# Performance work log

Hardware: AMD Instinct MI355X
Metric: run time of the kernel (lower is better)

Reference implementation:

```python
import math
import jax, jax.numpy as jnp
import numpy as np

BASE = 10000.0
SCALING_FACTOR = 1.0
ORIG_MAX_POS = 4096
BETA_FAST, BETA_SLOW = 32, 1
MSCALE = 0.707
MSCALE_ALL_DIM = 0.707


def _yarn_cos_sin(seq_len: int, dim: int):
    # DeepseekV3YarnRotaryEmbedding._set_cos_sin_cache, computed in numpy (constants)
    def corr_dim(num_rot):
        return dim * math.log(ORIG_MAX_POS / (num_rot * 2 * math.pi)) / (2 * math.log(BASE))
    low = max(math.floor(corr_dim(BETA_FAST)), 0)
    high = min(math.ceil(corr_dim(BETA_SLOW)), dim - 1)
    hi = high + 0.001 if low == high else high
    ramp = np.clip((np.arange(dim // 2, dtype=np.float32) - low) / (hi - low), 0.0, 1.0)
    inv_freq_mask = 1.0 - ramp
    freq_extra = 1.0 / BASE ** (np.arange(0, dim, 2, dtype=np.float32) / dim)
    freq_inter = freq_extra / SCALING_FACTOR
    inv_freq = freq_inter * (1.0 - inv_freq_mask) + freq_extra * inv_freq_mask
    t = np.arange(seq_len, dtype=np.float32)
    freqs = np.outer(t, inv_freq)
    def get_mscale(s, m):
        return 1.0 if s <= 1 else 0.1 * m * math.log(s) + 1.0
    _m = get_mscale(SCALING_FACTOR, MSCALE) / get_mscale(SCALING_FACTOR, MSCALE_ALL_DIM)
    emb = np.concatenate([freqs, freqs], axis=-1)  # [S, dim]
    return jnp.asarray(np.cos(emb) * _m), jnp.asarray(np.sin(emb) * _m)


def _rotate_half(x):
    x1, x2 = jnp.split(x, 2, axis=-1)
    return jnp.concatenate([-x2, x1], axis=-1)


def setup_inputs() -> dict:
    key = jax.random.key(0)
    ks = jax.random.split(key, 5)
    B, S, H, DN, DR, DV = 2, 2048, 16, 128, 64, 128
    return {
        "q_nope": jax.random.normal(ks[0], (B, S, H, DN), jnp.float32),
        "q_pe": jax.random.normal(ks[1], (B, S, H, DR), jnp.float32),
        "k_nope": jax.random.normal(ks[2], (B, S, H, DN), jnp.float32),
        "k_pe": jax.random.normal(ks[3], (B, S, 1, DR), jnp.float32),  # shared rope key head
        "v": jax.random.normal(ks[4], (B, S, H, DV), jnp.float32),
    }


def reference(q_nope, q_pe, k_nope, k_pe, v):
    B, S, H, DN = q_nope.shape
    DR = q_pe.shape[-1]
    sm_scale = (DN + DR) ** (-0.5)  # qk_head_dim**-0.5
    cos, sin = _yarn_cos_sin(S, DR)  # [S, DR]
    cos = cos[None, :, None, :]
    sin = sin[None, :, None, :]
    # decoupled RoPE on the rope slice (apply_rotary_pos_emb with position_ids=arange)
    qp = q_pe * cos + _rotate_half(q_pe) * sin              # [B,S,H,DR]
    kp = k_pe * cos + _rotate_half(k_pe) * sin              # [B,S,1,DR]
    kp = jnp.broadcast_to(kp, (B, S, H, DR))
    q = jnp.concatenate([q_nope, qp], axis=-1)              # [B,S,H,DN+DR]
    k = jnp.concatenate([k_nope, kp], axis=-1)
    # attention_ref: full fp32 logits, causal mask, lse*log2(e), softmax, PV
    logits = jnp.einsum('bmhd,bnhd->bhmn', q.astype(jnp.float32), k.astype(jnp.float32)) * sm_scale
    mask = jnp.arange(S)[:, None] >= jnp.arange(S)[None, :]  # qo_len == kv_len
    logits = jnp.where(mask[None, None], logits, -jnp.inf)
    lse = jnp.transpose(jax.scipy.special.logsumexp(logits, axis=-1), (0, 2, 1)) * math.log2(math.e)
    p = jax.nn.softmax(logits, axis=-1)
    o = jnp.einsum('bhmn,bnhd->bmhd', p, v.astype(jnp.float32))
    o = o.reshape(B * S, H, -1).astype(q_nope.dtype)        # [B*S, H, DV]
    return o, lse
```

## Files before the change

kernel.cpp:

```cpp
#include <hip/hip_runtime.h>
#include <hip/hip_bf16.h>
#include <math.h>

#define NB 2
#define SEQ 2048
#define NH 16
#define DNOPE 128
#define DROT 64
#define DVDIM 128
#define DQK 192
#define BM 64
#define BN 64

typedef __bf16 bf16x8_t __attribute__((ext_vector_type(8)));
typedef float f32x4_t __attribute__((ext_vector_type(4)));

#define LOG2_BASE_OVER_HALFDIM 0.41524101186092028f
#define KSL2 0.10412340175817158f
#define INV_2PI 0.15915494309189535f

#define KBF_ELEMS   ((size_t)NB * NH * SEQ * DQK)

#define KN_BLOCKS 4096
#define KR_BLOCKS 128
#define VPREP_BLOCKS 1024

__global__ __launch_bounds__(256) void prep_kernel(
    const float* __restrict__ k_nope, const float* __restrict__ k_pe,
    const float* __restrict__ v, __bf16* __restrict__ Kbf,
    __bf16* __restrict__ Vtb) {
  __shared__ __bf16 T[64][130];
  const int bid = blockIdx.x;
  const int tid = threadIdx.x;
  if (bid < KN_BLOCKS) {
    int gid = bid * 256 + tid;
    int d0 = (gid & 15) * 8;
    int rest = gid >> 4;
    int s = (rest >> 4) & (SEQ - 1);
    int h = rest & (NH - 1);
    int b = rest >> 15;
    const float* p = k_nope + ((size_t)((b * SEQ + s) * NH + h)) * DNOPE + d0;
    float4 a = *(const float4*)p;
    float4 c = *(const float4*)(p + 4);
    bf16x8_t o;
    o[0] = (__bf16)a.x; o[1] = (__bf16)a.y; o[2] = (__bf16)a.z; o[3] = (__bf16)a.w;
    o[4] = (__bf16)c.x; o[5] = (__bf16)c.y; o[6] = (__bf16)c.z; o[7] = (__bf16)c.w;
    *(bf16x8_t*)&Kbf[((size_t)(b * NH + h) * SEQ + s) * DQK + d0] = o;
  } else if (bid < KN_BLOCKS + KR_BLOCKS) {
    int gid = (bid - KN_BLOCKS) * 256 + tid;
    int dr0 = (gid & 7) * 8;
    int rest = gid >> 3;
    int s = rest & (SEQ - 1);
    int b = rest >> 11;
    const float* p = k_pe + (size_t)(b * SEQ + s) * DROT;
    float4 x0 = *(const float4*)(p + dr0);
    float4 x1 = *(const float4*)(p + dr0 + 4);
    int dro = (dr0 < 32) ? dr0 + 32 : dr0 - 32;
    float4 y0 = *(const float4*)(p + dro);
    float4 y1 = *(const float4*)(p + dro + 4);
    float sgn = (dr0 < 32) ? -1.0f : 1.0f;
    float xs[8] = {x0.x, x0.y, x0.z, x0.w, x1.x, x1.y, x1.z, x1.w};
    float ys[8] = {y0.x, y0.y, y0.z, y0.w, y1.x, y1.y, y1.z, y1.w};
    float invf0 = exp2f(-LOG2_BASE_OVER_HALFDIM * (float)(dr0 & 31));
    const float kj[8] = {
      1.0f,
      0.7499083907567589f,
      0.5624875938672282f,
      0.4219181499736729f,
      0.3163923045408737f,
      0.2372497216250197f,
      0.1779391804261401f,
      0.1334543036472316f};
    bf16x8_t o;
#pragma unroll
    for (int j = 0; j < 8; ++j) {
      float rev = (float)s * invf0 * (kj[j] * INV_2PI);
      rev = rev - floorf(rev);
      float sn = __builtin_amdgcn_sinf(rev);
      float cs = __builtin_amdgcn_cosf(rev);
      o[j] = (__bf16)(xs[j] * cs + sgn * ys[j] * sn);
    }
#pragma unroll
    for (int h = 0; h < NH; ++h)
      *(bf16x8_t*)&Kbf[((size_t)(b * NH + h) * SEQ + s) * DQK + DNOPE + dr0] = o;
  } else {
    int vb = bid - KN_BLOCKS - KR_BLOCKS;
    const int s0 = (vb & 31) * 64, h = (vb >> 5) & (NH - 1), b = vb >> 9;
#pragma unroll
    for (int r = 0; r < 8; ++r) {
      int task = tid + r * 256;
      int srow = task >> 5, c4 = (task & 31) * 4;
      const float* p = v + ((size_t)((b * SEQ + s0 + srow) * NH + h)) * DVDIM + c4;
      float4 a = *(const float4*)p;
      T[srow][c4 + 0] = (__bf16)a.x; T[srow][c4 + 1] = (__bf16)a.y;
      T[srow][c4 + 2] = (__bf16)a.z; T[srow][c4 + 3] = (__bf16)a.w;
    }
    __syncthreads();
#pragma unroll
    for (int r = 0; r < 4; ++r) {
      int task = tid + r * 256;
      int dv = task >> 3, c8 = (task & 7) * 8;
      bf16x8_t o;
#pragma unroll
      for (int u = 0; u < 8; ++u) o[u] = T[c8 + u][dv];
      *(bf16x8_t*)&Vtb[((size_t)(b * NH + h) * DVDIM + dv) * SEQ + s0 + c8] = o;
    }
  }
}

__global__ __launch_bounds__(256, 2) void mla_fwd_kernel(
    const float* __restrict__ q_nope, const float* __restrict__ q_pe,
    const __bf16* __restrict__ Kbf, const __bf16* __restrict__ Vtb,
    float* __restrict__ out_o, float* __restrict__ out_lse) {
  __shared__ __bf16 Kl[BN * DQK];
  __shared__ __bf16 Vl[DVDIM * BN];
  __shared__ __bf16 Pl[4 * 16 * BN];

  const int bx = blockIdx.x, h = blockIdx.y, b = blockIdx.z;
  const int tid = threadIdx.x;
  const int w = tid >> 6, lane = tid & 63;
  const int col = lane & 15, quad = lane >> 4;
  const int wm = w & 1;
  const int wnd = w >> 1;
  const int swz = col & 7;
  const int e0 = quad ^ swz, e1 = (quad + 4) ^ swz;

  const __bf16 onev = (col == 0) ? (__bf16)1.0f : (__bf16)0.0f;
  bf16x8_t vxf;
#pragma unroll
  for (int u = 0; u < 8; ++u) vxf[u] = onev;

  const __bf16* Kslab = Kbf + (size_t)(b * NH + h) * SEQ * DQK;
  const __bf16* Vslab = Vtb + (size_t)(b * NH + h) * DVDIM * SEQ;

  int kofs[6];
#pragma unroll
  for (int r = 0; r < 6; ++r) {
    int L = r * 256 + tid;
    int n = L / 24, jj = L - n * 24;
    int jsrc = (jj & ~7) | ((jj & 7) ^ (n & 7));
    kofs[r] = n * DQK + jsrc * 8;
  }
  int vofs[4];
#pragma unroll
  for (int r = 0; r < 4; ++r) {
    int L = r * 256 + tid;
    int dv = L >> 3, jj = L & 7;
    vofs[r] = dv * SEQ + (jj ^ (dv & 7)) * 8;
  }

  for (int half = 0; half < 2; ++half) {
    const int qt = half ? bx : (31 - bx);
    const int qb = qt * BM;

    bf16x8_t qf[2][6];
#pragma unroll
    for (int mt = 0; mt < 2; ++mt) {
      const int mrow = qb + wm * 32 + mt * 16 + col;
      const float* qn = q_nope + (size_t)((b * SEQ + mrow) * NH + h) * DNOPE;
      const float* qp = q_pe   + (size_t)((b * SEQ + mrow) * NH + h) * DROT;
#pragma unroll
      for (int c = 0; c < 4; ++c) {
        const float* p = qn + c * 32 + quad * 8;
        float4 a = *(const float4*)p;
        float4 bq = *(const float4*)(p + 4);
        bf16x8_t f;
        f[0]=(__bf16)(a.x*KSL2);  f[1]=(__bf16)(a.y*KSL2);
        f[2]=(__bf16)(a.z*KSL2);  f[3]=(__bf16)(a.w*KSL2);
        f[4]=(__bf16)(bq.x*KSL2); f[5]=(__bf16)(bq.y*KSL2);
        f[6]=(__bf16)(bq.z*KSL2); f[7]=(__bf16)(bq.w*KSL2);
        qf[mt][c] = f;
      }
      {
        const float* plo = qp + quad * 8;
        const float* phi = qp + 32 + quad * 8;
        float4 lo0 = *(const float4*)plo;
        float4 lo1 = *(const float4*)(plo + 4);
        float4 hi0 = *(const float4*)phi;
        float4 hi1 = *(const float4*)(phi + 4);
        float xl[8] = {lo0.x,lo0.y,lo0.z,lo0.w,lo1.x,lo1.y,lo1.z,lo1.w};
        float xh[8] = {hi0.x,hi0.y,hi0.z,hi0.w,hi1.x,hi1.y,hi1.z,hi1.w};
        bf16x8_t f4v, f5v;
#pragma unroll
        for (int j = 0; j < 8; ++j) {
          int i = quad * 8 + j;
          float invf = exp2f(-LOG2_BASE_OVER_HALFDIM * (float)i);
          float rev = (float)mrow * invf * INV_2PI;
          rev = rev - floorf(rev);
          float sn = __builtin_amdgcn_sinf(rev);
          float cs = __builtin_amdgcn_cosf(rev);
          f4v[j] = (__bf16)((xl[j] * cs - xh[j] * sn) * KSL2);
          f5v[j] = (__bf16)((xh[j] * cs + xl[j] * sn) * KSL2);
        }
        qf[mt][4] = f4v; qf[mt][5] = f5v;
      }
    }

    f32x4_t oacc[2][4];
#pragma unroll
    for (int mt = 0; mt < 2; ++mt)
#pragma unroll
      for (int d = 0; d < 4; ++d) oacc[mt][d] = (f32x4_t){0.f, 0.f, 0.f, 0.f};
    f32x4_t lacc[2];
    lacc[0] = (f32x4_t){0.f, 0.f, 0.f, 0.f};
    lacc[1] = (f32x4_t){0.f, 0.f, 0.f, 0.f};

    bf16x8_t Kreg[6], Vreg[4];
#pragma unroll
    for (int r = 0; r < 6; ++r) Kreg[r] = *(const bf16x8_t*)(Kslab + kofs[r]);
#pragma unroll
    for (int r = 0; r < 4; ++r) Vreg[r] = *(const bf16x8_t*)(Vslab + vofs[r]);

    for (int it = 0; it <= qt; ++it) {
      __syncthreads();
#pragma unroll
      for (int r = 0; r < 6; ++r) *(bf16x8_t*)&Kl[(r * 256 + tid) * 8] = Kreg[r];
#pragma unroll
      for (int r = 0; r < 4; ++r) *(bf16x8_t*)&Vl[(r * 256 + tid) * 8] = Vreg[r];
      __syncthreads();
      if (it < qt) {
        const __bf16* Ksrc = Kslab + (size_t)(it + 1) * BN * DQK;
        const __bf16* Vsrc = Vslab + (it + 1) * BN;
#pragma unroll
        for (int r = 0; r < 6; ++r) Kreg[r] = *(const bf16x8_t*)(Ksrc + kofs[r]);
#pragma unroll
        for (int r = 0; r < 4; ++r) Vreg[r] = *(const bf16x8_t*)(Vsrc + vofs[r]);
      }

      f32x4_t sacc[2][2];
#pragma unroll
      for (int mt = 0; mt < 2; ++mt)
#pragma unroll
        for (int nt = 0; nt < 2; ++nt) sacc[mt][nt] = (f32x4_t){0.f, 0.f, 0.f, 0.f};
#pragma unroll
      for (int nt = 0; nt < 2; ++nt) {
        const __bf16* kr = &Kl[(wnd * 32 + nt * 16 + col) * 24 * 8];
        bf16x8_t kf0 = *(const bf16x8_t*)&kr[e0 * 8];
        bf16x8_t kf1 = *(const bf16x8_t*)&kr[e1 * 8];
        bf16x8_t kf2 = *(const bf16x8_t*)&kr[64 + e0 * 8];
        bf16x8_t kf3 = *(const bf16x8_t*)&kr[64 + e1 * 8];
        bf16x8_t kf4 = *(const bf16x8_t*)&kr[128 + e0 * 8];
        bf16x8_t kf5 = *(const bf16x8_t*)&kr[128 + e1 * 8];
#pragma unroll
        for (int mt = 0; mt < 2; ++mt) {
          sacc[mt][nt] = __builtin_amdgcn_mfma_f32_16x16x32_bf16(qf[mt][0], kf0, sacc[mt][nt], 0, 0, 0);
          sacc[mt][nt] = __builtin_amdgcn_mfma_f32_16x16x32_bf16(qf[mt][1], kf1, sacc[mt][nt], 0, 0, 0);
          sacc[mt][nt] = __builtin_amdgcn_mfma_f32_16x16x32_bf16(qf[mt][2], kf2, sacc[mt][nt], 0, 0, 0);
          sacc[mt][nt] = __builtin_amdgcn_mfma_f32_16x16x32_bf16(qf[mt][3], kf3, sacc[mt][nt], 0, 0, 0);
          sacc[mt][nt] = __builtin_amdgcn_mfma_f32_16x16x32_bf16(qf[mt][4], kf4, sacc[mt][nt], 0, 0, 0);
          sacc[mt][nt] = __builtin_amdgcn_mfma_f32_16x16x32_bf16(qf[mt][5], kf5, sacc[mt][nt], 0, 0, 0);
        }
      }

      float pvv[2][2][4];
#pragma unroll
      for (int mt = 0; mt < 2; ++mt)
#pragma unroll
        for (int nt = 0; nt < 2; ++nt)
#pragma unroll
          for (int r = 0; r < 4; ++r) pvv[mt][nt][r] = exp2f(sacc[mt][nt][r]);
      if (it == qt) {
#pragma unroll
        for (int mt = 0; mt < 2; ++mt)
#pragma unroll
          for (int nt = 0; nt < 2; ++nt) {
            int nn = (it << 6) + wnd * 32 + nt * 16 + col;
#pragma unroll
            for (int r = 0; r < 4; ++r) {
              int mm = qb + wm * 32 + mt * 16 + quad * 4 + r;
              if (nn > mm) pvv[mt][nt][r] = 0.0f;
            }
          }
      }

#pragma unroll
      for (int mt = 0; mt < 2; ++mt) {
        __bf16* Pr = &Pl[(wm * 2 + mt) * 16 * BN];
#pragma unroll
        for (int nt = 0; nt < 2; ++nt)
#pragma unroll
          for (int r = 0; r < 4; ++r) {
            int row = quad * 4 + r;
            int j = wnd * 4 + nt * 2 + (col >> 3);
            Pr[(row * 8 + (j ^ (row & 7))) * 8 + (col & 7)] = (__bf16)pvv[mt][nt][r];
          }
      }
      __syncthreads();

      bf16x8_t pf0[2], pf1[2];
#pragma unroll
      for (int mt = 0; mt < 2; ++mt) {
        const __bf16* Pr = &Pl[(wm * 2 + mt) * 16 * BN];
        pf0[mt] = *(const bf16x8_t*)&Pr[(col * 8 + e0) * 8];
        pf1[mt] = *(const bf16x8_t*)&Pr[(col * 8 + e1) * 8];
      }
#pragma unroll
      for (int dt = 0; dt < 4; ++dt) {
        const __bf16* vr = &Vl[((wnd * 4 + dt) * 16 + col) * 64];
        bf16x8_t vf0 = *(const bf16x8_t*)&vr[e0 * 8];
        bf16x8_t vf1 = *(const bf16x8_t*)&vr[e1 * 8];
#pragma unroll
        for (int mt = 0; mt < 2; ++mt) {
          oacc[mt][dt] = __builtin_amdgcn_mfma_f32_16x16x32_bf16(pf0[mt], vf0, oacc[mt][dt], 0, 0, 0);
          oacc[mt][dt] = __builtin_amdgcn_mfma_f32_16x16x32_bf16(pf1[mt], vf1, oacc[mt][dt], 0, 0, 0);
        }
      }
#pragma unroll
      for (int mt = 0; mt < 2; ++mt) {
        lacc[mt] = __builtin_amdgcn_mfma_f32_16x16x32_bf16(pf0[mt], vxf, lacc[mt], 0, 0, 0);
        lacc[mt] = __builtin_amdgcn_mfma_f32_16x16x32_bf16(pf1[mt], vxf, lacc[mt], 0, 0, 0);
      }
    }

    float lr[2][4], inv_l[2][4];
#pragma unroll
    for (int mt = 0; mt < 2; ++mt)
#pragma unroll
      for (int r = 0; r < 4; ++r) {
        lr[mt][r] = __shfl(lacc[mt][r], lane & 48, 64);
        inv_l[mt][r] = 1.0f / lr[mt][r];
      }
#pragma unroll
    for (int mt = 0; mt < 2; ++mt)
#pragma unroll
      for (int dt = 0; dt < 4; ++dt)
#pragma unroll
        for (int r = 0; r < 4; ++r) {
          int mm = qb + wm * 32 + mt * 16 + quad * 4 + r;
          int dd = wnd * 64 + dt * 16 + col;
          out_o[(size_t)((b * SEQ + mm) * NH + h) * DVDIM + dd] =
              oacc[mt][dt][r] * inv_l[mt][r];
        }
    if (wnd == 0 && col < 4) {
#pragma unroll
      for (int mt = 0; mt < 2; ++mt) {
        int mm = qb + wm * 32 + mt * 16 + quad * 4 + col;
        out_lse[(size_t)(b * SEQ + mm) * NH + h] = log2f(lr[mt][col]);
      }
    }
  }
}

extern "C" void kernel_launch(void* const* d_in, const int* in_sizes, int n_in,
                              void* d_out, int out_size, void* d_ws, size_t ws_size,
                              hipStream_t stream) {
  const float* q_nope = (const float*)d_in[0];
  const float* q_pe   = (const float*)d_in[1];
  const float* k_nope = (const float*)d_in[2];
  const float* k_pe   = (const float*)d_in[3];
  const float* v      = (const float*)d_in[4];
  float* out_o   = (float*)d_out;
  float* out_lse = out_o + (size_t)NB * SEQ * NH * DVDIM;

  __bf16* Kbf = (__bf16*)d_ws;
  __bf16* Vtb = Kbf + KBF_ELEMS;

  prep_kernel<<<dim3(KN_BLOCKS + KR_BLOCKS + VPREP_BLOCKS), dim3(256), 0, stream>>>(
      k_nope, k_pe, v, Kbf, Vtb);
  mla_fwd_kernel<<<dim3(16, NH, NB), dim3(256), 0, stream>>>(
      q_nope, q_pe, Kbf, Vtb, out_o, out_lse);
}
```

Before: 232.2 us.

## Split PV over key halves per warp, removing mid-iteration block barrier

Each warp now multiplies its own 32-key slice of P by the full 128-wide V tile, using a private per-warp P buffer in shared memory. This removes the block-wide __syncthreads between writing and reading P in every KV iteration. The two partial O and row-sum accumulators are combined once at the end through a shared-memory reduction that reuses the K/V buffers. In exchange, O accumulator registers per thread double, which may raise register pressure or cause spills at two blocks per SM, and a reduction step with two extra barriers is added per query tile.

```diff
diff --git a/kernel.cpp b/kernel.cpp
--- a/kernel.cpp
+++ b/kernel.cpp
@@ -112,9 +112,12 @@
     const float* __restrict__ q_nope, const float* __restrict__ q_pe,
     const __bf16* __restrict__ Kbf, const __bf16* __restrict__ Vtb,
     float* __restrict__ out_o, float* __restrict__ out_lse) {
-  __shared__ __bf16 Kl[BN * DQK];
-  __shared__ __bf16 Vl[DVDIM * BN];
-  __shared__ __bf16 Pl[4 * 16 * BN];
+  __shared__ __align__(16) char smem[51200];
+  __bf16* Kl = (__bf16*)smem;
+  __bf16* Vl = (__bf16*)(smem + 24576);
+  __bf16* Pl = (__bf16*)(smem + 40960);
+  float*  Ored = (float*)smem;
+  float*  Lred = (float*)(smem + 64 * 132 * 4);
 
   const int bx = blockIdx.x, h = blockIdx.y, b = blockIdx.z;
   const int tid = threadIdx.x;
@@ -124,6 +127,7 @@
   const int wnd = w >> 1;
   const int swz = col & 7;
   const int e0 = quad ^ swz, e1 = (quad + 4) ^ swz;
+  const int ew = (wnd * 4 + quad) ^ swz;
 
   const __bf16 onev = (col == 0) ? (__bf16)1.0f : (__bf16)0.0f;
   bf16x8_t vxf;
@@ -148,6 +152,8 @@
     int dv = L >> 3, jj = L & 7;
     vofs[r] = dv * SEQ + (jj ^ (dv & 7)) * 8;
   }
+
+  __bf16* Pw = Pl + w * (32 * 40);
 
   for (int half = 0; half < 2; ++half) {
     const int qt = half ? bx : (31 - bx);
@@ -196,11 +202,11 @@
       }
     }
 
-    f32x4_t oacc[2][4];
+    f32x4_t oacc[2][8];
 #pragma unroll
     for (int mt = 0; mt < 2; ++mt)
 #pragma unroll
-      for (int d = 0; d < 4; ++d) oacc[mt][d] = (f32x4_t){0.f, 0.f, 0.f, 0.f};
+      for (int d = 0; d < 8; ++d) oacc[mt][d] = (f32x4_t){0.f, 0.f, 0.f, 0.f};
     f32x4_t lacc[2];
     lacc[0] = (f32x4_t){0.f, 0.f, 0.f, 0.f};
     lacc[1] = (f32x4_t){0.f, 0.f, 0.f, 0.f};
@@ -252,90 +258,84 @@
         }
       }
 
-      float pvv[2][2][4];
+      const bool dg = (it == qt);
 #pragma unroll
       for (int mt = 0; mt < 2; ++mt)
 #pragma unroll
         for (int nt = 0; nt < 2; ++nt)
 #pragma unroll
-          for (int r = 0; r < 4; ++r) pvv[mt][nt][r] = exp2f(sacc[mt][nt][r]);
-      if (it == qt) {
+          for (int r = 0; r < 4; ++r) {
+            float pe = exp2f(sacc[mt][nt][r]);
+            if (dg) {
+              int nn = (it << 6) + wnd * 32 + nt * 16 + col;
+              int mm = qb + wm * 32 + mt * 16 + quad * 4 + r;
+              if (nn > mm) pe = 0.0f;
+            }
+            Pw[(mt * 16 + quad * 4 + r) * 40 + nt * 16 + col] = (__bf16)pe;
+          }
+
+      bf16x8_t pa[2];
+#pragma unroll
+      for (int mt = 0; mt < 2; ++mt)
+        pa[mt] = *(const bf16x8_t*)&Pw[(mt * 16 + col) * 40 + quad * 8];
+#pragma unroll
+      for (int dt = 0; dt < 8; ++dt) {
+        bf16x8_t vf = *(const bf16x8_t*)&Vl[(dt * 16 + col) * 64 + ew * 8];
 #pragma unroll
         for (int mt = 0; mt < 2; ++mt)
-#pragma unroll
-          for (int nt = 0; nt < 2; ++nt) {
-            int nn = (it << 6) + wnd * 32 + nt * 16 + col;
-#pragma unroll
-            for (int r = 0; r < 4; ++r) {
-              int mm = qb + wm * 32 + mt * 16 + quad * 4 + r;
-              if (nn > mm) pvv[mt][nt][r] = 0.0f;
-            }
+          oacc[mt][dt] = __builtin_amdgcn_mfma_f32_16x16x32_bf16(pa[mt], vf, oacc[mt][dt], 0, 0, 0);
+      }
+#pragma unroll
+      for (int mt = 0; mt < 2; ++mt)
+        lacc[mt] = __builtin_amdgcn_mfma_f32_16x16x32_bf16(pa[mt], vxf, lacc[mt], 0, 0, 0);
+    }
+
+    __syncthreads();
+    if (wnd == 1) {
+#pragma unroll
+      for (int mt = 0; mt < 2; ++mt) {
+#pragma unroll
+        for (int dt = 0; dt < 8; ++dt)
+#pragma unroll
+          for (int r = 0; r < 4; ++r) {
+            int row = wm * 32 + mt * 16 + quad * 4 + r;
+            Ored[row * 132 + dt * 16 + col] = oacc[mt][dt][r];
           }
-      }
-
-#pragma unroll
-      for (int mt = 0; mt < 2; ++mt) {
-        __bf16* Pr = &Pl[(wm * 2 + mt) * 16 * BN];
-#pragma unroll
-        for (int nt = 0; nt < 2; ++nt)
+        if (col == 0)
+#pragma unroll
+          for (int r = 0; r < 4; ++r)
+            Lred[wm * 32 + mt * 16 + quad * 4 + r] = lacc[mt][r];
+      }
+    }
+    __syncthreads();
+    if (wnd == 0) {
+      float lr[2][4], inv_l[2][4];
+#pragma unroll
+      for (int mt = 0; mt < 2; ++mt)
+#pragma unroll
+        for (int r = 0; r < 4; ++r) {
+          float val = lacc[mt][r] + Lred[wm * 32 + mt * 16 + quad * 4 + r];
+          lr[mt][r] = __shfl(val, lane & 48, 64);
+          inv_l[mt][r] = 1.0f / lr[mt][r];
+        }
+#pragma unroll
+      for (int mt = 0; mt < 2; ++mt)
+#pragma unroll
+        for (int dt = 0; dt < 8; ++dt)
 #pragma unroll
           for (int r = 0; r < 4; ++r) {
-            int row = quad * 4 + r;
-            int j = wnd * 4 + nt * 2 + (col >> 3);
-            Pr[(row * 8 + (j ^ (row & 7))) * 8 + (col & 7)] = (__bf16)pvv[mt][nt][r];
+            int row = wm * 32 + mt * 16 + quad * 4 + r;
+            int mm = qb + row;
+            float sum = oacc[mt][dt][r] + Ored[row * 132 + dt * 16 + col];
+            out_o[(size_t)((b * SEQ + mm) * NH + h) * DVDIM + dt * 16 + col] =
+                sum * inv_l[mt][r];
           }
-      }
-      __syncthreads();
-
-      bf16x8_t pf0[2], pf1[2];
-#pragma unroll
-      for (int mt = 0; mt < 2; ++mt) {
-        const __bf16* Pr = &Pl[(wm * 2 + mt) * 16 * BN];
-        pf0[mt] = *(const bf16x8_t*)&Pr[(col * 8 + e0) * 8];
-        pf1[mt] = *(const bf16x8_t*)&Pr[(col * 8 + e1) * 8];
-      }
-#pragma unroll
-      for (int dt = 0; dt < 4; ++dt) {
-        const __bf16* vr = &Vl[((wnd * 4 + dt) * 16 + col) * 64];
-        bf16x8_t vf0 = *(const bf16x8_t*)&vr[e0 * 8];
-        bf16x8_t vf1 = *(const bf16x8_t*)&vr[e1 * 8];
+      if (col < 4) {
 #pragma unroll
         for (int mt = 0; mt < 2; ++mt) {
-          oacc[mt][dt] = __builtin_amdgcn_mfma_f32_16x16x32_bf16(pf0[mt], vf0, oacc[mt][dt], 0, 0, 0);
-          oacc[mt][dt] = __builtin_amdgcn_mfma_f32_16x16x32_bf16(pf1[mt], vf1, oacc[mt][dt], 0, 0, 0);
+          int mm = qb + wm * 32 + mt * 16 + quad * 4 + col;
+          out_lse[(size_t)(b * SEQ + mm) * NH + h] = log2f(lr[mt][col]);
         }
-      }
-#pragma unroll
-      for (int mt = 0; mt < 2; ++mt) {
-        lacc[mt] = __builtin_amdgcn_mfma_f32_16x16x32_bf16(pf0[mt], vxf, lacc[mt], 0, 0, 0);
-        lacc[mt] = __builtin_amdgcn_mfma_f32_16x16x32_bf16(pf1[mt], vxf, lacc[mt], 0, 0, 0);
-      }
-    }
-
-    float lr[2][4], inv_l[2][4];
-#pragma unroll
-    for (int mt = 0; mt < 2; ++mt)
-#pragma unroll
-      for (int r = 0; r < 4; ++r) {
-        lr[mt][r] = __shfl(lacc[mt][r], lane & 48, 64);
-        inv_l[mt][r] = 1.0f / lr[mt][r];
-      }
-#pragma unroll
-    for (int mt = 0; mt < 2; ++mt)
-#pragma unroll
-      for (int dt = 0; dt < 4; ++dt)
-#pragma unroll
-        for (int r = 0; r < 4; ++r) {
-          int mm = qb + wm * 32 + mt * 16 + quad * 4 + r;
-          int dd = wnd * 64 + dt * 16 + col;
-          out_o[(size_t)((b * SEQ + mm) * NH + h) * DVDIM + dd] =
-              oacc[mt][dt][r] * inv_l[mt][r];
-        }
-    if (wnd == 0 && col < 4) {
-#pragma unroll
-      for (int mt = 0; mt < 2; ++mt) {
-        int mm = qb + wm * 32 + mt * 16 + quad * 4 + col;
-        out_lse[(size_t)(b * SEQ + mm) * NH + h] = log2f(lr[mt][col]);
       }
     }
   }
```

New measurement: 240.0 us. 3.4% more time.

## Defer PV MFMA by one iteration with double-buffered V to drop a barrier

Applied to the files above, without the earlier changes.

Software-pipelines the attention loop so the P·V and row-sum MFMAs for tile it-1 run at the start of iteration it, reading a double-buffered V tile in shared memory. This removes one __syncthreads per iteration and lets the PV work overlap the K/V shared-memory stores. The last tile's PV is done in an epilogue after the loop. The exp and causal-mask step is also fused into the P store, and the extra V buffer adds 16 KB of LDS per block, which may affect occupancy.

```diff
diff --git a/kernel.cpp b/kernel.cpp
--- a/kernel.cpp
+++ b/kernel.cpp
@@ -113,7 +113,7 @@
     const __bf16* __restrict__ Kbf, const __bf16* __restrict__ Vtb,
     float* __restrict__ out_o, float* __restrict__ out_lse) {
   __shared__ __bf16 Kl[BN * DQK];
-  __shared__ __bf16 Vl[DVDIM * BN];
+  __shared__ __bf16 Vl[2][DVDIM * BN];
   __shared__ __bf16 Pl[4 * 16 * BN];
 
   const int bx = blockIdx.x, h = blockIdx.y, b = blockIdx.z;
@@ -213,10 +213,41 @@
 
     for (int it = 0; it <= qt; ++it) {
       __syncthreads();
+      bf16x8_t pf0[2], pf1[2];
+      if (it > 0) {
+#pragma unroll
+        for (int mt = 0; mt < 2; ++mt) {
+          const __bf16* Pr = &Pl[(wm * 2 + mt) * 16 * BN];
+          pf0[mt] = *(const bf16x8_t*)&Pr[(col * 8 + e0) * 8];
+          pf1[mt] = *(const bf16x8_t*)&Pr[(col * 8 + e1) * 8];
+        }
+      }
 #pragma unroll
       for (int r = 0; r < 6; ++r) *(bf16x8_t*)&Kl[(r * 256 + tid) * 8] = Kreg[r];
-#pragma unroll
-      for (int r = 0; r < 4; ++r) *(bf16x8_t*)&Vl[(r * 256 + tid) * 8] = Vreg[r];
+      {
+        __bf16* Vb = Vl[it & 1];
+#pragma unroll
+        for (int r = 0; r < 4; ++r) *(bf16x8_t*)&Vb[(r * 256 + tid) * 8] = Vreg[r];
+      }
+      if (it > 0) {
+        const __bf16* Vb = Vl[(it - 1) & 1];
+#pragma unroll
+        for (int dt = 0; dt < 4; ++dt) {
+          const __bf16* vr = &Vb[((wnd * 4 + dt) * 16 + col) * 64];
+          bf16x8_t vf0 = *(const bf16x8_t*)&vr[e0 * 8];
+          bf16x8_t vf1 = *(const bf16x8_t*)&vr[e1 * 8];
+#pragma unroll
+          for (int mt = 0; mt < 2; ++mt) {
+            oacc[mt][dt] = __builtin_amdgcn_mfma_f32_16x16x32_bf16(pf0[mt], vf0, oacc[mt][dt], 0, 0, 0);
+            oacc[mt][dt] = __builtin_amdgcn_mfma_f32_16x16x32_bf16(pf1[mt], vf1, oacc[mt][dt], 0, 0, 0);
+          }
+        }
+#pragma unroll
+        for (int mt = 0; mt < 2; ++mt) {
+          lacc[mt] = __builtin_amdgcn_mfma_f32_16x16x32_bf16(pf0[mt], vxf, lacc[mt], 0, 0, 0);
+          lacc[mt] = __builtin_amdgcn_mfma_f32_16x16x32_bf16(pf1[mt], vxf, lacc[mt], 0, 0, 0);
+        }
+      }
       __syncthreads();
       if (it < qt) {
         const __bf16* Ksrc = Kslab + (size_t)(it + 1) * BN * DQK;
@@ -252,27 +283,7 @@
         }
       }
 
-      float pvv[2][2][4];
-#pragma unroll
-      for (int mt = 0; mt < 2; ++mt)
-#pragma unroll
-        for (int nt = 0; nt < 2; ++nt)
-#pragma unroll
-          for (int r = 0; r < 4; ++r) pvv[mt][nt][r] = exp2f(sacc[mt][nt][r]);
-      if (it == qt) {
-#pragma unroll
-        for (int mt = 0; mt < 2; ++mt)
-#pragma unroll
-          for (int nt = 0; nt < 2; ++nt) {
-            int nn = (it << 6) + wnd * 32 + nt * 16 + col;
-#pragma unroll
-            for (int r = 0; r < 4; ++r) {
-              int mm = qb + wm * 32 + mt * 16 + quad * 4 + r;
-              if (nn > mm) pvv[mt][nt][r] = 0.0f;
-            }
-          }
-      }
-
+      const bool dg = (it == qt);
 #pragma unroll
       for (int mt = 0; mt < 2; ++mt) {
         __bf16* Pr = &Pl[(wm * 2 + mt) * 16 * BN];
@@ -280,13 +291,21 @@
         for (int nt = 0; nt < 2; ++nt)
 #pragma unroll
           for (int r = 0; r < 4; ++r) {
+            float pe = exp2f(sacc[mt][nt][r]);
+            if (dg) {
+              int nn = (it << 6) + wnd * 32 + nt * 16 + col;
+              int mm = qb + wm * 32 + mt * 16 + quad * 4 + r;
+              if (nn > mm) pe = 0.0f;
+            }
             int row = quad * 4 + r;
             int j = wnd * 4 + nt * 2 + (col >> 3);
-            Pr[(row * 8 + (j ^ (row & 7))) * 8 + (col & 7)] = (__bf16)pvv[mt][nt][r];
+            Pr[(row * 8 + (j ^ (row & 7))) * 8 + (col & 7)] = (__bf16)pe;
           }
       }
-      __syncthreads();
-
+    }
+
+    __syncthreads();
+    {
       bf16x8_t pf0[2], pf1[2];
 #pragma unroll
       for (int mt = 0; mt < 2; ++mt) {
@@ -294,9 +313,10 @@
         pf0[mt] = *(const bf16x8_t*)&Pr[(col * 8 + e0) * 8];
         pf1[mt] = *(const bf16x8_t*)&Pr[(col * 8 + e1) * 8];
       }
+      const __bf16* Vb = Vl[qt & 1];
 #pragma unroll
       for (int dt = 0; dt < 4; ++dt) {
-        const __bf16* vr = &Vl[((wnd * 4 + dt) * 16 + col) * 64];
+        const __bf16* vr = &Vb[((wnd * 4 + dt) * 16 + col) * 64];
         bf16x8_t vf0 = *(const bf16x8_t*)&vr[e0 * 8];
         bf16x8_t vf1 = *(const bf16x8_t*)&vr[e1 * 8];
 #pragma unroll
```

New measurement: 285.5 us. 23.0% more time.

## Use direct global-to-LDS loads with double-buffered V tiles

Applied to the files above, without the earlier changes.

Replaces register-staged K/V prefetch with global_load_lds async copies straight into shared memory. V is double-buffered so the next tile can load while PV runs, and K is overwritten after the QK stage finishes. This removes the register staging, the LDS store pass and one barrier per iteration, and adds 16KB of LDS. No explicit vmcnt wait appears before the next iteration reads the asynchronously loaded LDS data, so correctness depends on the compiler inserting waits.

```diff
diff --git a/kernel.cpp b/kernel.cpp
--- a/kernel.cpp
+++ b/kernel.cpp
@@ -18,6 +18,11 @@
 #define LOG2_BASE_OVER_HALFDIM 0.41524101186092028f
 #define KSL2 0.10412340175817158f
 #define INV_2PI 0.15915494309189535f
+
+typedef __attribute__((address_space(1))) unsigned int as1_uint;
+typedef __attribute__((address_space(3))) unsigned int as3_uint;
+#define GLOAD16(g, l)                                                        \
+  __builtin_amdgcn_global_load_lds((as1_uint*)(g), (as3_uint*)(l), 16, 0, 0)
 
 #define KBF_ELEMS   ((size_t)NB * NH * SEQ * DQK)
 
@@ -113,7 +118,8 @@
     const __bf16* __restrict__ Kbf, const __bf16* __restrict__ Vtb,
     float* __restrict__ out_o, float* __restrict__ out_lse) {
   __shared__ __bf16 Kl[BN * DQK];
-  __shared__ __bf16 Vl[DVDIM * BN];
+  __shared__ __bf16 Vl0[DVDIM * BN];
+  __shared__ __bf16 Vl1[DVDIM * BN];
   __shared__ __bf16 Pl[4 * 16 * BN];
 
   const int bx = blockIdx.x, h = blockIdx.y, b = blockIdx.z;
@@ -124,6 +130,7 @@
   const int wnd = w >> 1;
   const int swz = col & 7;
   const int e0 = quad ^ swz, e1 = (quad + 4) ^ swz;
+  const int wb = w * 512;
 
   const __bf16 onev = (col == 0) ? (__bf16)1.0f : (__bf16)0.0f;
   bf16x8_t vxf;
@@ -152,6 +159,12 @@
   for (int half = 0; half < 2; ++half) {
     const int qt = half ? bx : (31 - bx);
     const int qb = qt * BM;
+
+    __syncthreads();
+#pragma unroll
+    for (int r = 0; r < 6; ++r) GLOAD16(Kslab + kofs[r], &Kl[r * 2048 + wb]);
+#pragma unroll
+    for (int r = 0; r < 4; ++r) GLOAD16(Vslab + vofs[r], &Vl0[r * 2048 + wb]);
 
     bf16x8_t qf[2][6];
 #pragma unroll
@@ -205,27 +218,8 @@
     lacc[0] = (f32x4_t){0.f, 0.f, 0.f, 0.f};
     lacc[1] = (f32x4_t){0.f, 0.f, 0.f, 0.f};
 
-    bf16x8_t Kreg[6], Vreg[4];
-#pragma unroll
-    for (int r = 0; r < 6; ++r) Kreg[r] = *(const bf16x8_t*)(Kslab + kofs[r]);
-#pragma unroll
-    for (int r = 0; r < 4; ++r) Vreg[r] = *(const bf16x8_t*)(Vslab + vofs[r]);
-
-    for (int it = 0; it <= qt; ++it) {
+    auto do_iter = [&](int it, const __bf16* Vcur, __bf16* Vnext) {
       __syncthreads();
-#pragma unroll
-      for (int r = 0; r < 6; ++r) *(bf16x8_t*)&Kl[(r * 256 + tid) * 8] = Kreg[r];
-#pragma unroll
-      for (int r = 0; r < 4; ++r) *(bf16x8_t*)&Vl[(r * 256 + tid) * 8] = Vreg[r];
-      __syncthreads();
-      if (it < qt) {
-        const __bf16* Ksrc = Kslab + (size_t)(it + 1) * BN * DQK;
-        const __bf16* Vsrc = Vslab + (it + 1) * BN;
-#pragma unroll
-        for (int r = 0; r < 6; ++r) Kreg[r] = *(const bf16x8_t*)(Ksrc + kofs[r]);
-#pragma unroll
-        for (int r = 0; r < 4; ++r) Vreg[r] = *(const bf16x8_t*)(Vsrc + vofs[r]);
-      }
 
       f32x4_t sacc[2][2];
 #pragma unroll
@@ -252,27 +246,7 @@
         }
       }
 
-      float pvv[2][2][4];
-#pragma unroll
-      for (int mt = 0; mt < 2; ++mt)
-#pragma unroll
-        for (int nt = 0; nt < 2; ++nt)
-#pragma unroll
-          for (int r = 0; r < 4; ++r) pvv[mt][nt][r] = exp2f(sacc[mt][nt][r]);
-      if (it == qt) {
-#pragma unroll
-        for (int mt = 0; mt < 2; ++mt)
-#pragma unroll
-          for (int nt = 0; nt < 2; ++nt) {
-            int nn = (it << 6) + wnd * 32 + nt * 16 + col;
-#pragma unroll
-            for (int r = 0; r < 4; ++r) {
-              int mm = qb + wm * 32 + mt * 16 + quad * 4 + r;
-              if (nn > mm) pvv[mt][nt][r] = 0.0f;
-            }
-          }
-      }
-
+      const bool dg = (it == qt);
 #pragma unroll
       for (int mt = 0; mt < 2; ++mt) {
         __bf16* Pr = &Pl[(wm * 2 + mt) * 16 * BN];
@@ -280,12 +254,27 @@
         for (int nt = 0; nt < 2; ++nt)
 #pragma unroll
           for (int r = 0; r < 4; ++r) {
+            float pe = exp2f(sacc[mt][nt][r]);
+            if (dg) {
+              int nn = (it << 6) + wnd * 32 + nt * 16 + col;
+              int mm = qb + wm * 32 + mt * 16 + quad * 4 + r;
+              if (nn > mm) pe = 0.0f;
+            }
             int row = quad * 4 + r;
             int j = wnd * 4 + nt * 2 + (col >> 3);
-            Pr[(row * 8 + (j ^ (row & 7))) * 8 + (col & 7)] = (__bf16)pvv[mt][nt][r];
+            Pr[(row * 8 + (j ^ (row & 7))) * 8 + (col & 7)] = (__bf16)pe;
           }
       }
       __syncthreads();
+
+      if (it < qt) {
+        const __bf16* Ksrc = Kslab + (size_t)(it + 1) * BN * DQK;
+        const __bf16* Vsrc = Vslab + (it + 1) * BN;
+#pragma unroll
+        for (int r = 0; r < 6; ++r) GLOAD16(Ksrc + kofs[r], &Kl[r * 2048 + wb]);
+#pragma unroll
+        for (int r = 0; r < 4; ++r) GLOAD16(Vsrc + vofs[r], &Vnext[r * 2048 + wb]);
+      }
 
       bf16x8_t pf0[2], pf1[2];
 #pragma unroll
@@ -296,7 +285,7 @@
       }
 #pragma unroll
       for (int dt = 0; dt < 4; ++dt) {
-        const __bf16* vr = &Vl[((wnd * 4 + dt) * 16 + col) * 64];
+        const __bf16* vr = &Vcur[((wnd * 4 + dt) * 16 + col) * 64];
         bf16x8_t vf0 = *(const bf16x8_t*)&vr[e0 * 8];
         bf16x8_t vf1 = *(const bf16x8_t*)&vr[e1 * 8];
 #pragma unroll
@@ -310,6 +299,11 @@
         lacc[mt] = __builtin_amdgcn_mfma_f32_16x16x32_bf16(pf0[mt], vxf, lacc[mt], 0, 0, 0);
         lacc[mt] = __builtin_amdgcn_mfma_f32_16x16x32_bf16(pf1[mt], vxf, lacc[mt], 0, 0, 0);
       }
+    };
+
+    for (int it = 0; it <= qt; it += 2) {
+      do_iter(it, Vl0, Vl1);
+      if (it + 1 <= qt) do_iter(it + 1, Vl1, Vl0);
     }
 
     float lr[2][4], inv_l[2][4];
```

Measured after the change: 228.3 us. Within noise of the previous version (-1.7%).
